# Kernel tuning notes

Measured on AMD Instinct MI355X. Metric: run time of the kernel, lower is better.

Reference implementation:

```python
import jax, jax.numpy as jnp
import numpy as np

NUM_BASIS = 10
CUTOFF = 1.0
SQRT3 = 3.0 ** 0.5
SMOOTH_C = 1.14136 * float(np.exp(2.0))  # e3nn smooth_finite constant


def soft_unit_step(x):
    # e3nn soft_unit_step: exp(-1/x) for x>0 else 0 (nan-safe for grads)
    xs = jnp.where(x > 0, x, 1.0)
    return jnp.where(x > 0, jnp.exp(-1.0 / xs), 0.0)


def smooth_finite_embed(length):
    # soft_one_hot_linspace(start=0, end=cutoff, number=NUM_BASIS,
    #                       basis='smooth_finite', cutoff=True), then * sqrt(NUM_BASIS)
    values = jnp.linspace(0.0, CUTOFF, NUM_BASIS + 2)
    step = values[1] - values[0]
    values = values[1:-1]                      # [NUM_BASIS]
    diff = (length[:, None] - values) / step   # [E, NUM_BASIS]
    f = SMOOTH_C * soft_unit_step(diff + 1.0) * soft_unit_step(1.0 - diff)
    return f * (NUM_BASIS ** 0.5)


def sh_lmax2_norm(vec):
    # e3nn o3.spherical_harmonics(lmax=2, normalize=True, normalization='norm')
    r = jnp.linalg.norm(vec, axis=-1, keepdims=True)
    u = vec / jnp.where(r > 0, r, 1.0)
    x, y, z = u[:, 0], u[:, 1], u[:, 2]
    sh0 = jnp.ones_like(x)                       # l=0
    sh2_0 = SQRT3 * x * z                        # l=2 block ('norm' normalized)
    sh2_1 = SQRT3 * x * y
    sh2_2 = y * y - 0.5 * (x * x + z * z)
    sh2_3 = SQRT3 * y * z
    sh2_4 = (SQRT3 / 2.0) * (z * z - x * x)
    return jnp.stack([sh0, x, y, z, sh2_0, sh2_1, sh2_2, sh2_3, sh2_4], axis=-1)


def setup_inputs() -> dict:
    key = jax.random.key(0)
    k1, k2, k3, k4 = jax.random.split(key, 4)
    pos = jax.random.uniform(k1, (100000, 3), dtype=jnp.float32)
    query_pos = jax.random.uniform(k2, (8, 1250, 3), dtype=jnp.float32)
    # Surrogate for torch_cluster.radius(x, y, r=1.2*cutoff): fixed-size edge list
    edge_src = jax.random.randint(k3, (4000000,), 0, 10000)   # indexes flattened queries
    edge_dst = jax.random.randint(k4, (4000000,), 0, 100000)  # indexes points
    return {"pos": pos, "query_pos": query_pos, "edge_src": edge_src, "edge_dst": edge_dst}


def reference(pos, query_pos, edge_src, edge_dst):
    y = query_pos.reshape(-1, 3)                 # [Nt*Ny, 3]
    edge_vec = y[edge_src] - pos[edge_dst]       # [E, 3] irregular gather
    edge_length = jnp.linalg.norm(edge_vec, axis=-1)
    edge_length_embedded = smooth_finite_embed(edge_length)  # [E, 10]
    edge_sh = sh_lmax2_norm(edge_vec)                         # [E, 9]
    return edge_sh, edge_length_embedded
```

## Files before the change

### kernel.cpp

```cpp
#include <hip/hip_runtime.h>


#define SQRT3F 1.7320508075688772f
#define EMB_K 26.6692997f

__global__ __launch_bounds__(256) void qsh_kernel(
    const float* __restrict__ pos,
    const float* __restrict__ qpos,
    const int* __restrict__ esrc,
    const int* __restrict__ edst,
    float* __restrict__ out_sh,
    float* __restrict__ out_emb,
    int n)
{
    __shared__ float lds[256 * 19];

    const int tid  = threadIdx.x;
    const int base = blockIdx.x * 256;
    const int e    = base + tid;
    const int count = min(256, n - base);

    if (tid < count) {
        int s = esrc[e];
        int d = edst[e];

        float ax = qpos[3 * s + 0];
        float ay = qpos[3 * s + 1];
        float az = qpos[3 * s + 2];
        float bx = pos[3 * d + 0];
        float by = pos[3 * d + 1];
        float bz = pos[3 * d + 2];

        float vx = ax - bx, vy = ay - by, vz = az - bz;
        float r2 = vx * vx + vy * vy + vz * vz;
        float r = sqrtf(r2);
        float inv = (r > 0.0f) ? (1.0f / r) : 1.0f;
        float x = vx * inv, y = vy * inv, z = vz * inv;

        float* l = lds + tid * 19;
        l[0] = 1.0f;
        l[1] = x;
        l[2] = y;
        l[3] = z;
        l[4] = SQRT3F * x * z;
        l[5] = SQRT3F * x * y;
        l[6] = y * y - 0.5f * (x * x + z * z);
        l[7] = SQRT3F * y * z;
        l[8] = 0.5f * SQRT3F * (z * z - x * x);

        float t = r * 11.0f;
#pragma unroll
        for (int i = 0; i < 10; ++i) {
            float a = t - (float)i;
            float b = (float)(i + 2) - t;
            float f = 0.0f;
            if (a > 0.0f && b > 0.0f) {
                f = EMB_K * __expf(-(__frcp_rn(a) + __frcp_rn(b)));
            }
            l[9 + i] = f;
        }
    }
    __syncthreads();

    float* osh = out_sh + (size_t)base * 9;
    float* oem = out_emb + (size_t)base * 10;

    if (count == 256) {
#pragma unroll
        for (int k = 0; k < 9; ++k) {
            int idx = k * 256 + tid;
            int ee = idx / 9;
            int c  = idx - ee * 9;
            osh[idx] = lds[ee * 19 + c];
        }
#pragma unroll
        for (int k = 0; k < 10; ++k) {
            int idx = k * 256 + tid;
            int ee = idx / 10;
            int c  = idx - ee * 10;
            oem[idx] = lds[ee * 19 + 9 + c];
        }
    } else {
        int nsh = count * 9;
        for (int idx = tid; idx < nsh; idx += 256) {
            int ee = idx / 9;
            int c  = idx - ee * 9;
            osh[idx] = lds[ee * 19 + c];
        }
        int nem = count * 10;
        for (int idx = tid; idx < nem; idx += 256) {
            int ee = idx / 10;
            int c  = idx - ee * 10;
            oem[idx] = lds[ee * 19 + 9 + c];
        }
    }
}

extern "C" void kernel_launch(void* const* d_in, const int* in_sizes, int n_in,
                              void* d_out, int out_size, void* d_ws, size_t ws_size,
                              hipStream_t stream) {
    const float* pos  = (const float*)d_in[0];
    const float* qpos = (const float*)d_in[1];
    const int* esrc = (const int*)d_in[2];
    const int* edst = (const int*)d_in[3];
    int n = in_sizes[2];

    float* out_sh  = (float*)d_out;
    float* out_emb = out_sh + (size_t)n * 9;

    int block = 256;
    int grid = (n + block - 1) / block;
    qsh_kernel<<<grid, block, 0, stream>>>(pos, qpos, esrc, edst, out_sh, out_emb, n);
}
```

Baseline: 375.2 us.

## Pad point coordinates to float4, process two edges per thread, nontemporal IO

```diff
diff --git a/kernel.cpp b/kernel.cpp
--- a/kernel.cpp
+++ b/kernel.cpp
@@ -3,61 +3,91 @@
 
 #define SQRT3F 1.7320508075688772f
 #define EMB_K 26.6692997f
+#define TPB 256
+#define EPB 512
 
+__global__ __launch_bounds__(256) void pad_kernel(
+    const float* __restrict__ pos, const float* __restrict__ qpos,
+    float4* __restrict__ pos4, float4* __restrict__ qpos4,
+    int npos, int nq)
+{
+    int i = blockIdx.x * blockDim.x + threadIdx.x;
+    if (i < npos)
+        pos4[i] = make_float4(pos[3 * i + 0], pos[3 * i + 1], pos[3 * i + 2], 0.f);
+    if (i < nq)
+        qpos4[i] = make_float4(qpos[3 * i + 0], qpos[3 * i + 1], qpos[3 * i + 2], 0.f);
+}
+
+__device__ __forceinline__ void compute_edge(
+    float ax, float ay, float az, float bx, float by, float bz,
+    float* __restrict__ l)
+{
+    float vx = ax - bx, vy = ay - by, vz = az - bz;
+    float r2 = vx * vx + vy * vy + vz * vz;
+    float r = sqrtf(r2);
+    float inv = (r > 0.f) ? (1.f / r) : 1.f;
+    float x = vx * inv, y = vy * inv, z = vz * inv;
+
+    l[0] = 1.f;
+    l[1] = x;
+    l[2] = y;
+    l[3] = z;
+    l[4] = SQRT3F * x * z;
+    l[5] = SQRT3F * x * y;
+    l[6] = y * y - 0.5f * (x * x + z * z);
+    l[7] = SQRT3F * y * z;
+    l[8] = 0.5f * SQRT3F * (z * z - x * x);
+
+#pragma unroll
+    for (int j = 0; j < 10; ++j) l[9 + j] = 0.f;
+    float t = r * 11.f;
+    int k = (int)t;
+#pragma unroll
+    for (int m = 0; m < 2; ++m) {
+        int j = k - 1 + m;
+        float a = t - (float)j;
+        float b = (float)(j + 2) - t;
+        if (j >= 0 && j < 10 && a > 0.f && b > 0.f)
+            l[9 + j] = EMB_K * __expf(-(__frcp_rn(a) + __frcp_rn(b)));
+    }
+}
+
+template <bool PAD>
 __global__ __launch_bounds__(256) void qsh_kernel(
     const float* __restrict__ pos,
     const float* __restrict__ qpos,
+    const float4* __restrict__ pos4,
+    const float4* __restrict__ qpos4,
     const int* __restrict__ esrc,
     const int* __restrict__ edst,
     float* __restrict__ out_sh,
     float* __restrict__ out_emb,
     int n)
 {
-    __shared__ float lds[256 * 19];
+    __shared__ float lds[EPB * 19];
 
-    const int tid  = threadIdx.x;
-    const int base = blockIdx.x * 256;
-    const int e    = base + tid;
-    const int count = min(256, n - base);
+    const int tid = threadIdx.x;
+    const int base = blockIdx.x * EPB;
+    const int count = min(EPB, n - base);
 
-    if (tid < count) {
-        int s = esrc[e];
-        int d = edst[e];
-
-        float ax = qpos[3 * s + 0];
-        float ay = qpos[3 * s + 1];
-        float az = qpos[3 * s + 2];
-        float bx = pos[3 * d + 0];
-        float by = pos[3 * d + 1];
-        float bz = pos[3 * d + 2];
-
-        float vx = ax - bx, vy = ay - by, vz = az - bz;
-        float r2 = vx * vx + vy * vy + vz * vz;
-        float r = sqrtf(r2);
-        float inv = (r > 0.0f) ? (1.0f / r) : 1.0f;
-        float x = vx * inv, y = vy * inv, z = vz * inv;
-
-        float* l = lds + tid * 19;
-        l[0] = 1.0f;
-        l[1] = x;
-        l[2] = y;
-        l[3] = z;
-        l[4] = SQRT3F * x * z;
-        l[5] = SQRT3F * x * y;
-        l[6] = y * y - 0.5f * (x * x + z * z);
-        l[7] = SQRT3F * y * z;
-        l[8] = 0.5f * SQRT3F * (z * z - x * x);
-
-        float t = r * 11.0f;
 #pragma unroll
-        for (int i = 0; i < 10; ++i) {
-            float a = t - (float)i;
-            float b = (float)(i + 2) - t;
-            float f = 0.0f;
-            if (a > 0.0f && b > 0.0f) {
-                f = EMB_K * __expf(-(__frcp_rn(a) + __frcp_rn(b)));
+    for (int m = 0; m < 2; ++m) {
+        int le = tid + m * TPB;
+        if (le < count) {
+            int e = base + le;
+            int s = __builtin_nontemporal_load(esrc + e);
+            int d = __builtin_nontemporal_load(edst + e);
+            float ax, ay, az, bx, by, bz;
+            if (PAD) {
+                float4 q = qpos4[s];
+                float4 p = pos4[d];
+                ax = q.x; ay = q.y; az = q.z;
+                bx = p.x; by = p.y; bz = p.z;
+            } else {
+                ax = qpos[3 * s + 0]; ay = qpos[3 * s + 1]; az = qpos[3 * s + 2];
+                bx = pos[3 * d + 0];  by = pos[3 * d + 1];  bz = pos[3 * d + 2];
             }
-            l[9 + i] = f;
+            compute_edge(ax, ay, az, bx, by, bz, lds + le * 19);
         }
     }
     __syncthreads();
@@ -65,33 +95,33 @@
     float* osh = out_sh + (size_t)base * 9;
     float* oem = out_emb + (size_t)base * 10;
 
-    if (count == 256) {
+    if (count == EPB) {
 #pragma unroll
-        for (int k = 0; k < 9; ++k) {
-            int idx = k * 256 + tid;
+        for (int k2 = 0; k2 < 18; ++k2) {
+            int idx = k2 * TPB + tid;
             int ee = idx / 9;
-            int c  = idx - ee * 9;
-            osh[idx] = lds[ee * 19 + c];
+            int c = idx - ee * 9;
+            __builtin_nontemporal_store(lds[ee * 19 + c], osh + idx);
         }
 #pragma unroll
-        for (int k = 0; k < 10; ++k) {
-            int idx = k * 256 + tid;
+        for (int k2 = 0; k2 < 20; ++k2) {
+            int idx = k2 * TPB + tid;
             int ee = idx / 10;
-            int c  = idx - ee * 10;
-            oem[idx] = lds[ee * 19 + 9 + c];
+            int c = idx - ee * 10;
+            __builtin_nontemporal_store(lds[ee * 19 + 9 + c], oem + idx);
         }
     } else {
         int nsh = count * 9;
-        for (int idx = tid; idx < nsh; idx += 256) {
+        for (int idx = tid; idx < nsh; idx += TPB) {
             int ee = idx / 9;
-            int c  = idx - ee * 9;
-            osh[idx] = lds[ee * 19 + c];
+            int c = idx - ee * 9;
+            __builtin_nontemporal_store(lds[ee * 19 + c], osh + idx);
         }
         int nem = count * 10;
-        for (int idx = tid; idx < nem; idx += 256) {
+        for (int idx = tid; idx < nem; idx += TPB) {
             int ee = idx / 10;
-            int c  = idx - ee * 10;
-            oem[idx] = lds[ee * 19 + 9 + c];
+            int c = idx - ee * 10;
+            __builtin_nontemporal_store(lds[ee * 19 + 9 + c], oem + idx);
         }
     }
 }
@@ -103,12 +133,25 @@
     const float* qpos = (const float*)d_in[1];
     const int* esrc = (const int*)d_in[2];
     const int* edst = (const int*)d_in[3];
-    int n = in_sizes[2];
+    int npos = in_sizes[0] / 3;
+    int nq   = in_sizes[1] / 3;
+    int n    = in_sizes[2];
 
     float* out_sh  = (float*)d_out;
     float* out_emb = out_sh + (size_t)n * 9;
 
-    int block = 256;
-    int grid = (n + block - 1) / block;
-    qsh_kernel<<<grid, block, 0, stream>>>(pos, qpos, esrc, edst, out_sh, out_emb, n);
+    int grid = (n + EPB - 1) / EPB;
+
+    size_t need = ((size_t)npos + (size_t)nq) * sizeof(float4);
+    if (ws_size >= need) {
+        float4* pos4  = (float4*)d_ws;
+        float4* qpos4 = pos4 + npos;
+        int pgrid = (max(npos, nq) + TPB - 1) / TPB;
+        pad_kernel<<<pgrid, TPB, 0, stream>>>(pos, qpos, pos4, qpos4, npos, nq);
+        qsh_kernel<true><<<grid, TPB, 0, stream>>>(
+            pos, qpos, pos4, qpos4, esrc, edst, out_sh, out_emb, n);
+    } else {
+        qsh_kernel<false><<<grid, TPB, 0, stream>>>(
+            pos, qpos, nullptr, nullptr, esrc, edst, out_sh, out_emb, n);
+    }
 }
```

Result: faster. 361.1 us (-3.8%).
